# Optimization experiments

Measured on AMD Instinct MI355X. Metric: run time of the kernel, lower is better.

## Reference

```python
import jax, jax.numpy as jnp
import numpy as np

MARGIN_1 = 1.0
MARGIN_2 = 1.5
ALPHA_1 = 2.4
ALPHA_2 = 2.2
TVAL = 1.0
EPS = 1e-5


def setup_inputs() -> dict:
    key = jax.random.key(0)
    k1, k2, k3 = jax.random.split(key, 3)
    N, D = 4096, 2048
    x = jax.random.normal(k1, (N, D), dtype=jnp.float32)
    targets = jax.random.randint(k2, (N,), 0, 128, dtype=jnp.int32)
    sub = jax.random.randint(k3, (N,), 0, 2, dtype=jnp.int32)
    return {"x": x, "targets": targets, "sub": sub}


def _euclidean_dist(x):
    # pairwise distances of rows, clamped like torch .clamp(min=1e-12).sqrt()
    sq = jnp.sum(x * x, axis=1)  # [N]
    d2 = sq[:, None] + sq[None, :] - 2.0 * (x @ x.T)
    return jnp.sqrt(jnp.maximum(d2, 1e-12))  # [N, N]


def reference(x, targets, sub):
    # L2 normalize rows (norm=True path)
    x = x / jnp.maximum(jnp.linalg.norm(x, axis=1, keepdims=True), 1e-12)
    dist = _euclidean_dist(x)  # [N, N]
    N = dist.shape[0]

    eye = jnp.eye(N, dtype=bool)
    same_id = targets[:, None] == targets[None, :]
    is_pos = same_id & ~eye
    is_neg = ~same_id
    intra = sub[:, None] == sub[None, :]

    m_pos_intra = is_pos & intra
    m_pos_cross = is_pos & ~intra
    m_neg_intra = is_neg & intra
    m_neg_cross = is_neg & ~intra

    def ap_term(mask, margin, alpha):
        vals = jnp.maximum(dist + (margin - alpha), 0.0)
        cnt = jnp.sum(mask, axis=1).astype(dist.dtype)
        return jnp.sum(jnp.where(mask, vals, 0.0), axis=1) / (cnt + EPS)

    def an_term(mask, alpha):
        sel = mask & (dist < alpha)
        diff = alpha - dist  # = (alpha - d); weight = exp(tval * diff)
        w = jnp.where(sel, jnp.exp(TVAL * diff), 0.0)
        num = jnp.sum(jnp.where(sel, diff, 0.0) * w, axis=1)
        den = jnp.sum(w, axis=1) + EPS
        return num / den

    loss_rows = (
        ap_term(m_pos_intra, MARGIN_1, ALPHA_1)
        + ap_term(m_pos_cross, MARGIN_2, ALPHA_2)
        + an_term(m_neg_intra, ALPHA_1)
        + an_term(m_neg_cross, ALPHA_2)
    )
    return jnp.sum(loss_rows) / N
```

## Files before the change

### kernel.cpp

```cpp
#include <hip/hip_runtime.h>
#include <math.h>

#define THREADS 256
#define GT 512
#define BM 128
#define QBK 64
#define EPSV 1e-5f
#define C1E 11.023176380641601f
#define C2E 9.025013499434122f
#define FP8_SCALE 256.0f
#define INV_SCALE2 1.52587890625e-5f

typedef float f32x4 __attribute__((ext_vector_type(4)));

__launch_bounds__(THREADS)
__global__ void norm_conv_fp8_kernel(const float* __restrict__ x,
                                     unsigned char* __restrict__ xq, int D) {
    const int row = blockIdx.x;
    const float4* x4 = (const float4*)(x + (size_t)row * D);
    const int tid = threadIdx.x;

    float s = 0.f;
    for (int b = tid * 2; b * 4 < D; b += THREADS * 2) {
        float4 v0 = x4[b];
        float4 v1 = x4[b + 1];
        s += v0.x * v0.x + v0.y * v0.y + v0.z * v0.z + v0.w * v0.w
           + v1.x * v1.x + v1.y * v1.y + v1.z * v1.z + v1.w * v1.w;
    }
#pragma unroll
    for (int off = 32; off > 0; off >>= 1) s += __shfl_down(s, off, 64);
    __shared__ float red[THREADS / 64 + 1];
    if ((tid & 63) == 0) red[tid >> 6] = s;
    __syncthreads();
    if (tid == 0) {
        float tot = 0.f;
#pragma unroll
        for (int w = 0; w < THREADS / 64; ++w) tot += red[w];
        red[THREADS / 64] = FP8_SCALE / fmaxf(sqrtf(tot), 1e-12f);
    }
    __syncthreads();
    const float sc = red[THREADS / 64];

    int2* out = (int2*)(xq + (size_t)row * D);
    for (int b = tid * 2; b * 4 < D; b += THREADS * 2) {
        float4 v0 = x4[b];
        float4 v1 = x4[b + 1];
        int lo = __builtin_amdgcn_cvt_pk_fp8_f32(v0.x * sc, v0.y * sc, 0, 0);
        lo = __builtin_amdgcn_cvt_pk_fp8_f32(v0.z * sc, v0.w * sc, lo, 1);
        int hi = __builtin_amdgcn_cvt_pk_fp8_f32(v1.x * sc, v1.y * sc, 0, 0);
        hi = __builtin_amdgcn_cvt_pk_fp8_f32(v1.z * sc, v1.w * sc, hi, 1);
        int2 o; o.x = lo; o.y = hi;
        out[b >> 1] = o;
    }
}

__global__ void row_inv_norm_kernel(const float* __restrict__ x,
                                    float* __restrict__ inv_norm, int D) {
    const int row = blockIdx.x;
    const float4* x4 = (const float4*)(x + (size_t)row * D);
    const int nf4 = D >> 2;
    float s = 0.f;
    for (int i = threadIdx.x; i < nf4; i += THREADS) {
        float4 v = x4[i];
        s += v.x * v.x + v.y * v.y + v.z * v.z + v.w * v.w;
    }
#pragma unroll
    for (int off = 32; off > 0; off >>= 1) s += __shfl_down(s, off, 64);
    __shared__ float red[THREADS / 64];
    if ((threadIdx.x & 63) == 0) red[threadIdx.x >> 6] = s;
    __syncthreads();
    if (threadIdx.x == 0) {
        float tot = 0.f;
#pragma unroll
        for (int w = 0; w < THREADS / 64; ++w) tot += red[w];
        inv_norm[row] = 1.0f / fmaxf(sqrtf(tot), 1e-12f);
    }
}

#define GLDS16(g, l)                                                          \
    __builtin_amdgcn_global_load_lds(                                         \
        (const __attribute__((address_space(1))) unsigned int*)(g),           \
        (__attribute__((address_space(3))) unsigned int*)(l), 16, 0, 0)

__launch_bounds__(GT, 6)
__global__ void gram_fp8_kernel(const unsigned char* __restrict__ xq,
                                const int* __restrict__ targets,
                                const int* __restrict__ sub,
                                float* __restrict__ pr,
                                float* __restrict__ pc,
                                int D) {
    __shared__ unsigned char As[2][BM * QBK];
    __shared__ unsigned char Bs[2][BM * QBK];

    int tk = blockIdx.x;
    if ((gridDim.x & 7) == 0) {
        const int per = gridDim.x >> 3;
        tk = (tk & 7) * per + (tk >> 3);
    }

    int bx = (int)((sqrtf(8.0f * tk + 1.0f) - 1.0f) * 0.5f);
    while ((bx + 1) * (bx + 2) / 2 <= tk) ++bx;
    while (bx * (bx + 1) / 2 > tk) --bx;
    const int by = tk - bx * (bx + 1) / 2;

    const int tid = threadIdx.x;
    const int w = tid >> 6;
    const int lane = tid & 63;
    const int wm = w >> 2;
    const int wn = w & 3;
    const int quad = lane >> 4;
    const int cl = lane & 15;

    const int rowA0 = by * BM;
    const int colB0 = bx * BM;

    const int r0 = tid >> 2;
    const int qs = (tid & 3) ^ ((tid >> 3) & 3);
    const unsigned char* sA = xq + (size_t)(rowA0 + r0) * D + qs * 16;
    const unsigned char* sB = xq + (size_t)(colB0 + r0) * D + qs * 16;
    const int dof = w * 1024;

    int aoff[4], boff[2];
#pragma unroll
    for (int mi = 0; mi < 4; ++mi) {
        const int ar = wm * 64 + mi * 16 + cl;
        aoff[mi] = ar * QBK + ((((quad >> 1) ^ ((ar >> 1) & 3)) << 4))
                 + ((quad & 1) << 3);
    }
#pragma unroll
    for (int ni = 0; ni < 2; ++ni) {
        const int br = wn * 32 + ni * 16 + cl;
        boff[ni] = br * QBK + ((((quad >> 1) ^ ((br >> 1) & 3)) << 4))
                 + ((quad & 1) << 3);
    }

    f32x4 accv[4][2];
#pragma unroll
    for (int mi = 0; mi < 4; ++mi)
#pragma unroll
        for (int ni = 0; ni < 2; ++ni) accv[mi][ni] = (f32x4)(0.f);

    const int nIter = D / QBK;

    GLDS16(sA, &As[0][0] + dof);
    GLDS16(sB, &Bs[0][0] + dof);
    __syncthreads();

    for (int it = 0; it < nIter; ++it) {
        const int cur = it & 1;
        const int nxt = cur ^ 1;

        if (it + 1 < nIter) {
            const int kb = (it + 1) * QBK;
            GLDS16(sA + kb, &As[nxt][0] + dof);
            GLDS16(sB + kb, &Bs[nxt][0] + dof);
        }

        long af[4], bfv[2];
#pragma unroll
        for (int mi = 0; mi < 4; ++mi)
            af[mi] = *(const long*)&As[cur][aoff[mi]];
#pragma unroll
        for (int ni = 0; ni < 2; ++ni)
            bfv[ni] = *(const long*)&Bs[cur][boff[ni]];
#pragma unroll
        for (int mi = 0; mi < 4; ++mi)
#pragma unroll
            for (int ni = 0; ni < 2; ++ni)
                accv[mi][ni] = __builtin_amdgcn_mfma_f32_16x16x32_fp8_fp8(
                    af[mi], bfv[ni], accv[mi][ni], 0, 0, 0);
#pragma unroll
        for (int mi = 0; mi < 4; ++mi)
            af[mi] = *(const long*)&As[cur][aoff[mi] ^ 32];
#pragma unroll
        for (int ni = 0; ni < 2; ++ni)
            bfv[ni] = *(const long*)&Bs[cur][boff[ni] ^ 32];
#pragma unroll
        for (int mi = 0; mi < 4; ++mi)
#pragma unroll
            for (int ni = 0; ni < 2; ++ni)
                accv[mi][ni] = __builtin_amdgcn_mfma_f32_16x16x32_fp8_fp8(
                    af[mi], bfv[ni], accv[mi][ni], 0, 0, 0);

        __syncthreads();
    }

    int tj[2], sj[2];
#pragma unroll
    for (int ni = 0; ni < 2; ++ni) {
        const int gc = colB0 + wn * 32 + ni * 16 + cl;
        tj[ni] = targets[gc];
        sj[ni] = sub[gc];
    }

    float* rowp = (float*)&As[0][0];
#pragma unroll
    for (int mi = 0; mi < 4; ++mi) {
#pragma unroll
        for (int r = 0; r < 4; ++r) {
            const int rloc = wm * 64 + mi * 16 + quad * 4 + r;
            const int gi = rowA0 + rloc;
            const int ti = targets[gi];
            const int si = sub[gi];

            float s0 = 0.f, s1 = 0.f, s2 = 0.f, s3 = 0.f;
            float s4 = 0.f, s5 = 0.f, s6 = 0.f, s7 = 0.f;
#pragma unroll
            for (int ni = 0; ni < 2; ++ni) {
                const int gj = colB0 + wn * 32 + ni * 16 + cl;
                const float d2 =
                    fmaf(-2.0f * INV_SCALE2, accv[mi][ni][r], 2.0f);
                const float dd = sqrtf(fmaxf(d2, 1e-12f));
                accv[mi][ni][r] = dd;
                const bool same = (ti == tj[ni]);
                const bool intra = (si == sj[ni]);
                const bool pos = same && (gi != gj);
                const bool neg = !same;
                const float mg = intra ? 1.4f : 0.7f;
                const float v = fmaxf(dd - mg, 0.f);
                const float e = __expf(-dd);
                const float de = dd * e;
                if (pos && intra)  { s0 += v;  s1 += 1.f; }
                if (pos && !intra) { s2 += v;  s3 += 1.f; }
                if (neg && intra)  { s4 += de; s5 += e; }
                if (neg && !intra) { s6 += de; s7 += e; }
            }
#pragma unroll
            for (int off = 1; off < 16; off <<= 1) {
                s0 += __shfl_xor(s0, off, 64);
                s1 += __shfl_xor(s1, off, 64);
                s2 += __shfl_xor(s2, off, 64);
                s3 += __shfl_xor(s3, off, 64);
                s4 += __shfl_xor(s4, off, 64);
                s5 += __shfl_xor(s5, off, 64);
                s6 += __shfl_xor(s6, off, 64);
                s7 += __shfl_xor(s7, off, 64);
            }
            if (cl == 0) {
                float* dst = rowp + ((wn << 7) + rloc) * 8;
                float4 p0 = {s0, s1, s2, s3};
                float4 p1 = {s4, s5, s6, s7};
                *(float4*)(dst) = p0;
                *(float4*)(dst + 4) = p1;
            }
        }
    }
    __syncthreads();
    {
        const size_t prbase = (size_t)tk * 1024;
        for (int i = tid; i < 1024; i += GT)
            pr[prbase + i] = rowp[i] + rowp[1024 + i]
                           + rowp[2048 + i] + rowp[3072 + i];
    }

    float* colp = (float*)&Bs[0][0];
#pragma unroll
    for (int ni = 0; ni < 2; ++ni) {
        const int gj = colB0 + wn * 32 + ni * 16 + cl;
        const int tjc = tj[ni];
        const int sjc = sj[ni];
        float s0 = 0.f, s1 = 0.f, s2 = 0.f, s3 = 0.f;
        float s4 = 0.f, s5 = 0.f, s6 = 0.f, s7 = 0.f;
#pragma unroll
        for (int mi = 0; mi < 4; ++mi) {
#pragma unroll
            for (int r = 0; r < 4; ++r) {
                const int gi = rowA0 + wm * 64 + mi * 16 + quad * 4 + r;
                const int ti = targets[gi];
                const int si = sub[gi];
                const float dd = accv[mi][ni][r];
                const bool same = (ti == tjc);
                const bool intra = (si == sjc);
                const bool pos = same && (gi != gj);
                const bool neg = !same;
                const float mg = intra ? 1.4f : 0.7f;
                const float v = fmaxf(dd - mg, 0.f);
                const float e = __expf(-dd);
                const float de = dd * e;
                if (pos && intra)  { s0 += v;  s1 += 1.f; }
                if (pos && !intra) { s2 += v;  s3 += 1.f; }
                if (neg && intra)  { s4 += de; s5 += e; }
                if (neg && !intra) { s6 += de; s7 += e; }
            }
        }
        s0 += __shfl_xor(s0, 16, 64); s0 += __shfl_xor(s0, 32, 64);
        s1 += __shfl_xor(s1, 16, 64); s1 += __shfl_xor(s1, 32, 64);
        s2 += __shfl_xor(s2, 16, 64); s2 += __shfl_xor(s2, 32, 64);
        s3 += __shfl_xor(s3, 16, 64); s3 += __shfl_xor(s3, 32, 64);
        s4 += __shfl_xor(s4, 16, 64); s4 += __shfl_xor(s4, 32, 64);
        s5 += __shfl_xor(s5, 16, 64); s5 += __shfl_xor(s5, 32, 64);
        s6 += __shfl_xor(s6, 16, 64); s6 += __shfl_xor(s6, 32, 64);
        s7 += __shfl_xor(s7, 16, 64); s7 += __shfl_xor(s7, 32, 64);
        if (lane < 16) {
            const int colloc = wn * 32 + ni * 16 + lane;
            float* dst = colp + ((wm << 7) + colloc) * 8;
            float4 p0 = {s0, s1, s2, s3};
            float4 p1 = {s4, s5, s6, s7};
            *(float4*)(dst) = p0;
            *(float4*)(dst + 4) = p1;
        }
    }
    __syncthreads();
    {
        const float om = (bx == by) ? 0.f : 1.f;
        const size_t pcbase = (size_t)tk * 1024;
        for (int i = tid; i < 1024; i += GT)
            pc[pcbase + i] = (colp[i] + colp[1024 + i]) * om;
    }
}

__global__ void finalize_sym_kernel(const float* __restrict__ pr,
                                    const float* __restrict__ pc,
                                    float* __restrict__ out, int N, int nbx) {
    const int tid = threadIdx.x;
    const int rloc16 = tid >> 4;
    const int st = tid & 15;
    const int i = blockIdx.x * 16 + rloc16;
    const int B = i >> 7;
    const int rl = i & 127;
    const int nrow = nbx - B;
    const int ntot = nbx + 1;

    float a0 = 0.f, a1 = 0.f, a2 = 0.f, a3 = 0.f;
    float a4 = 0.f, a5 = 0.f, a6 = 0.f, a7 = 0.f;
    for (int s = st; s < ntot; s += 16) {
        const float* base;
        if (s < nrow) {
            const int bxx = B + s;
            base = pr + ((size_t)(bxx * (bxx + 1) / 2 + B) * 128 + rl) * 8;
        } else {
            const int byy = s - nrow;
            base = pc + ((size_t)(B * (B + 1) / 2 + byy) * 128 + rl) * 8;
        }
        float4 u0 = *(const float4*)(base);
        float4 u1 = *(const float4*)(base + 4);
        a0 += u0.x; a1 += u0.y; a2 += u0.z; a3 += u0.w;
        a4 += u1.x; a5 += u1.y; a6 += u1.z; a7 += u1.w;
    }
#pragma unroll
    for (int off = 1; off < 16; off <<= 1) {
        a0 += __shfl_xor(a0, off, 64);
        a1 += __shfl_xor(a1, off, 64);
        a2 += __shfl_xor(a2, off, 64);
        a3 += __shfl_xor(a3, off, 64);
        a4 += __shfl_xor(a4, off, 64);
        a5 += __shfl_xor(a5, off, 64);
        a6 += __shfl_xor(a6, off, 64);
        a7 += __shfl_xor(a7, off, 64);
    }
    __shared__ float lred[16];
    if (st == 0) {
        const float l = a0 / (a1 + EPSV) + a2 / (a3 + EPSV)
            + (C1E * fmaf(2.4f, a5, -a4)) / (C1E * a5 + EPSV)
            + (C2E * fmaf(2.2f, a7, -a6)) / (C2E * a7 + EPSV);
        lred[rloc16] = l;
    }
    __syncthreads();
    if (tid == 0) {
        float tot = 0.f;
#pragma unroll
        for (int k2 = 0; k2 < 16; ++k2) tot += lred[k2];
        atomicAdd(out, tot / (float)N);
    }
}

__launch_bounds__(THREADS, 2)
__global__ void dist_loss_kernel(const float* __restrict__ x,
                                 const int* __restrict__ targets,
                                 const int* __restrict__ sub,
                                 const float* __restrict__ inv_norm,
                                 float* __restrict__ acc,
                                 int N, int D) {
    __shared__ float Asf[16][128];
    __shared__ float Bsf[16][128];

    const int nbx = N / 128;
    const int bx = blockIdx.x % nbx;
    const int by = blockIdx.x / nbx;
    const int tid = threadIdx.x;
    const int tx = tid & 15;
    const int ty = tid >> 4;
    const int rowA0 = by * 128;
    const int colB0 = bx * 128;
    const float* Abase = x + (size_t)rowA0 * D;
    const float* Bbase = x + (size_t)colB0 * D;

    float accv[8][8];
#pragma unroll
    for (int r = 0; r < 8; ++r)
#pragma unroll
        for (int c = 0; c < 8; ++c) accv[r][c] = 0.f;

    for (int kb = 0; kb < D; kb += 16) {
#pragma unroll
        for (int l = 0; l < 2; ++l) {
            const int f = tid + l * THREADS;
            const int row = f >> 2;
            const int kq = (f & 3) << 2;
            float4 va = *(const float4*)(Abase + (size_t)row * D + kb + kq);
            float4 vb = *(const float4*)(Bbase + (size_t)row * D + kb + kq);
            Asf[kq + 0][row] = va.x; Asf[kq + 1][row] = va.y;
            Asf[kq + 2][row] = va.z; Asf[kq + 3][row] = va.w;
            Bsf[kq + 0][row] = vb.x; Bsf[kq + 1][row] = vb.y;
            Bsf[kq + 2][row] = vb.z; Bsf[kq + 3][row] = vb.w;
        }
        __syncthreads();
#pragma unroll
        for (int k = 0; k < 16; ++k) {
            float4 a0 = *(const float4*)&Asf[k][ty * 8];
            float4 a1 = *(const float4*)&Asf[k][ty * 8 + 4];
            float4 b0 = *(const float4*)&Bsf[k][tx * 8];
            float4 b1 = *(const float4*)&Bsf[k][tx * 8 + 4];
            float ar[8] = {a0.x, a0.y, a0.z, a0.w, a1.x, a1.y, a1.z, a1.w};
            float br[8] = {b0.x, b0.y, b0.z, b0.w, b1.x, b1.y, b1.z, b1.w};
#pragma unroll
            for (int r = 0; r < 8; ++r)
#pragma unroll
                for (int c = 0; c < 8; ++c)
                    accv[r][c] = fmaf(ar[r], br[c], accv[r][c]);
        }
        __syncthreads();
    }

    const int row_base = rowA0 + ty * 8;
    const int col_base = colB0 + tx * 8;
    int tjc[8], sjc[8];
    float invj[8];
#pragma unroll
    for (int c = 0; c < 8; ++c) {
        tjc[c] = targets[col_base + c];
        sjc[c] = sub[col_base + c];
        invj[c] = inv_norm[col_base + c];
    }
#pragma unroll
    for (int r = 0; r < 8; ++r) {
        const int gi = row_base + r;
        const int ti = targets[gi];
        const int si = sub[gi];
        const float invi = inv_norm[gi];
        float s0 = 0.f, s1 = 0.f, s2 = 0.f, s3 = 0.f;
        float s4 = 0.f, s5 = 0.f, s6 = 0.f, s7 = 0.f;
#pragma unroll
        for (int c = 0; c < 8; ++c) {
            const int gj = col_base + c;
            const float dot = accv[r][c] * invi * invj[c];
            const float dd = sqrtf(fmaxf(2.f - 2.f * dot, 1e-12f));
            const bool same = (ti == tjc[c]);
            const bool intra = (si == sjc[c]);
            const bool pos = same && (gi != gj);
            const bool neg = !same;
            const float df = (intra ? 2.4f : 2.2f) - dd;
            const float wgt = __expf(df);
            const float v = fmaxf(dd - (intra ? 1.4f : 0.7f), 0.f);
            if (pos && intra)  { s0 += v; s1 += 1.f; }
            if (pos && !intra) { s2 += v; s3 += 1.f; }
            if (neg && intra)  { s4 += df * wgt; s5 += wgt; }
            if (neg && !intra) { s6 += df * wgt; s7 += wgt; }
        }
#pragma unroll
        for (int off = 1; off < 16; off <<= 1) {
            s0 += __shfl_xor(s0, off, 64);
            s1 += __shfl_xor(s1, off, 64);
            s2 += __shfl_xor(s2, off, 64);
            s3 += __shfl_xor(s3, off, 64);
            s4 += __shfl_xor(s4, off, 64);
            s5 += __shfl_xor(s5, off, 64);
            s6 += __shfl_xor(s6, off, 64);
            s7 += __shfl_xor(s7, off, 64);
        }
        if (tx == 0) {
            float* a = acc + (size_t)gi * 8;
            atomicAdd(a + 0, s0); atomicAdd(a + 1, s1);
            atomicAdd(a + 2, s2); atomicAdd(a + 3, s3);
            atomicAdd(a + 4, s4); atomicAdd(a + 5, s5);
            atomicAdd(a + 6, s6); atomicAdd(a + 7, s7);
        }
    }
}

__global__ void finalize_kernel(const float* __restrict__ acc,
                                float* __restrict__ out, int N) {
    float s = 0.f;
    for (int i = threadIdx.x; i < N; i += THREADS) {
        const float* a = acc + (size_t)i * 8;
        s += a[0] / (a[1] + EPSV) + a[2] / (a[3] + EPSV)
           + a[4] / (a[5] + EPSV) + a[6] / (a[7] + EPSV);
    }
#pragma unroll
    for (int off = 32; off > 0; off >>= 1) s += __shfl_down(s, off, 64);
    __shared__ float red[THREADS / 64];
    if ((threadIdx.x & 63) == 0) red[threadIdx.x >> 6] = s;
    __syncthreads();
    if (threadIdx.x == 0) {
        float tot = 0.f;
#pragma unroll
        for (int w = 0; w < THREADS / 64; ++w) tot += red[w];
        out[0] = tot / (float)N;
    }
}

extern "C" void kernel_launch(void* const* d_in, const int* in_sizes, int n_in,
                              void* d_out, int out_size, void* d_ws, size_t ws_size,
                              hipStream_t stream) {
    const float* x = (const float*)d_in[0];
    const int* targets = (const int*)d_in[1];
    const int* sub = (const int*)d_in[2];
    const int N = in_sizes[1];
    const int D = in_sizes[0] / N;

    const int nbx = N / BM;
    const int T = nbx * (nbx + 1) / 2;
    const size_t sliceB = (size_t)T * 128 * 8 * sizeof(float);
    const size_t need = (size_t)N * D + 2 * sliceB;

    if (ws_size >= need) {
        unsigned char* xq = (unsigned char*)d_ws;
        float* pr = (float*)((char*)d_ws + (size_t)N * D);
        float* pc = pr + (size_t)T * 128 * 8;

        hipMemsetAsync(d_out, 0, sizeof(float), stream);
        norm_conv_fp8_kernel<<<N, THREADS, 0, stream>>>(x, xq, D);
        gram_fp8_kernel<<<T, GT, 0, stream>>>(xq, targets, sub, pr, pc, D);
        finalize_sym_kernel<<<N / 16, THREADS, 0, stream>>>(
            pr, pc, (float*)d_out, N, nbx);
    } else {
        float* inv_norm = (float*)d_ws;
        float* acc = inv_norm + N;
        hipMemsetAsync(acc, 0, (size_t)N * 8 * sizeof(float), stream);
        row_inv_norm_kernel<<<N, THREADS, 0, stream>>>(x, inv_norm, D);
        dist_loss_kernel<<<nbx * nbx, THREADS, 0, stream>>>(
            x, targets, sub, inv_norm, acc, N, D);
        finalize_kernel<<<1, THREADS, 0, stream>>>(acc, (float*)d_out, N);
    }
}
```

Measured before the change: 179.7 us.

## Use 4-wave 64x64 warp tiles with triple-buffered LDS and vmcnt-based pipelining

The fp8 Gram kernel drops from 8 waves to 4 waves per 128x128 tile, so each wave computes a 64x64 sub-tile (4x4 MFMA blocks), which raises register reuse of the A/B fragments. The LDS ring grows from double to triple buffering, with loads issued two stages ahead and synchronised by explicit s_waitcnt vmcnt plus a barrier, replacing the per-iteration __syncthreads. Row targets and sub values are preloaded into registers once. The cost is more accumulator registers per thread and lower occupancy (launch bounds 256 threads, 3 blocks per CU), and the hand-written waitcnt assumes a fixed count of outstanding loads.

```diff
diff --git a/kernel.cpp b/kernel.cpp
--- a/kernel.cpp
+++ b/kernel.cpp
@@ -2,7 +2,6 @@
 #include <math.h>
 
 #define THREADS 256
-#define GT 512
 #define BM 128
 #define QBK 64
 #define EPSV 1e-5f
@@ -82,15 +81,15 @@
         (const __attribute__((address_space(1))) unsigned int*)(g),           \
         (__attribute__((address_space(3))) unsigned int*)(l), 16, 0, 0)
 
-__launch_bounds__(GT, 6)
+__launch_bounds__(THREADS, 3)
 __global__ void gram_fp8_kernel(const unsigned char* __restrict__ xq,
                                 const int* __restrict__ targets,
                                 const int* __restrict__ sub,
                                 float* __restrict__ pr,
                                 float* __restrict__ pc,
                                 int D) {
-    __shared__ unsigned char As[2][BM * QBK];
-    __shared__ unsigned char Bs[2][BM * QBK];
+    __shared__ unsigned char As[3][BM * QBK];
+    __shared__ unsigned char Bs[3][BM * QBK];
 
     int tk = blockIdx.x;
     if ((gridDim.x & 7) == 0) {
@@ -106,91 +105,122 @@
     const int tid = threadIdx.x;
     const int w = tid >> 6;
     const int lane = tid & 63;
-    const int wm = w >> 2;
-    const int wn = w & 3;
+    const int wm = w >> 1;
+    const int wn = w & 1;
     const int quad = lane >> 4;
     const int cl = lane & 15;
 
     const int rowA0 = by * BM;
     const int colB0 = bx * BM;
 
-    const int r0 = tid >> 2;
     const int qs = (tid & 3) ^ ((tid >> 3) & 3);
-    const unsigned char* sA = xq + (size_t)(rowA0 + r0) * D + qs * 16;
-    const unsigned char* sB = xq + (size_t)(colB0 + r0) * D + qs * 16;
-    const int dof = w * 1024;
-
-    int aoff[4], boff[2];
+    const unsigned char* sA[2];
+    const unsigned char* sB[2];
+    int dof[2];
+#pragma unroll
+    for (int l = 0; l < 2; ++l) {
+        const int r = l * 64 + (tid >> 2);
+        sA[l] = xq + (size_t)(rowA0 + r) * D + qs * 16;
+        sB[l] = xq + (size_t)(colB0 + r) * D + qs * 16;
+        dof[l] = (l * 256 + w * 64) * 16;
+    }
+
+    int aoff[4], boff[4];
 #pragma unroll
     for (int mi = 0; mi < 4; ++mi) {
         const int ar = wm * 64 + mi * 16 + cl;
-        aoff[mi] = ar * QBK + ((((quad >> 1) ^ ((ar >> 1) & 3)) << 4))
+        aoff[mi] = ar * QBK + (((quad >> 1) ^ ((ar >> 1) & 3)) << 4)
                  + ((quad & 1) << 3);
     }
 #pragma unroll
-    for (int ni = 0; ni < 2; ++ni) {
-        const int br = wn * 32 + ni * 16 + cl;
-        boff[ni] = br * QBK + ((((quad >> 1) ^ ((br >> 1) & 3)) << 4))
+    for (int ni = 0; ni < 4; ++ni) {
+        const int br = wn * 64 + ni * 16 + cl;
+        boff[ni] = br * QBK + (((quad >> 1) ^ ((br >> 1) & 3)) << 4)
                  + ((quad & 1) << 3);
     }
 
-    f32x4 accv[4][2];
+    f32x4 accv[4][4];
 #pragma unroll
     for (int mi = 0; mi < 4; ++mi)
 #pragma unroll
-        for (int ni = 0; ni < 2; ++ni) accv[mi][ni] = (f32x4)(0.f);
+        for (int ni = 0; ni < 4; ++ni) accv[mi][ni] = (f32x4)(0.f);
 
     const int nIter = D / QBK;
 
-    GLDS16(sA, &As[0][0] + dof);
-    GLDS16(sB, &Bs[0][0] + dof);
-    __syncthreads();
-
-    for (int it = 0; it < nIter; ++it) {
-        const int cur = it & 1;
-        const int nxt = cur ^ 1;
-
-        if (it + 1 < nIter) {
-            const int kb = (it + 1) * QBK;
-            GLDS16(sA + kb, &As[nxt][0] + dof);
-            GLDS16(sB + kb, &Bs[nxt][0] + dof);
-        }
-
-        long af[4], bfv[2];
+#pragma unroll
+    for (int l = 0; l < 2; ++l) {
+        GLDS16(sA[l], &As[0][0] + dof[l]);
+        GLDS16(sB[l], &Bs[0][0] + dof[l]);
+    }
+#pragma unroll
+    for (int l = 0; l < 2; ++l) {
+        GLDS16(sA[l] + QBK, &As[1][0] + dof[l]);
+        GLDS16(sB[l] + QBK, &Bs[1][0] + dof[l]);
+    }
+
+    int cs = 0;
+    int ps = 2;
+    for (int t = 0; t < nIter; ++t) {
+        if (t + 1 < nIter)
+            asm volatile("s_waitcnt vmcnt(4)" ::: "memory");
+        else
+            asm volatile("s_waitcnt vmcnt(0)" ::: "memory");
+        __builtin_amdgcn_s_barrier();
+
+        if (t + 2 < nIter) {
+            const int kb = (t + 2) * QBK;
+#pragma unroll
+            for (int l = 0; l < 2; ++l) {
+                GLDS16(sA[l] + kb, &As[ps][0] + dof[l]);
+                GLDS16(sB[l] + kb, &Bs[ps][0] + dof[l]);
+            }
+        }
+
+        const unsigned char* Ac = &As[cs][0];
+        const unsigned char* Bc = &Bs[cs][0];
+        long af[4], bf[4];
 #pragma unroll
         for (int mi = 0; mi < 4; ++mi)
-            af[mi] = *(const long*)&As[cur][aoff[mi]];
-#pragma unroll
-        for (int ni = 0; ni < 2; ++ni)
-            bfv[ni] = *(const long*)&Bs[cur][boff[ni]];
+            af[mi] = *(const long*)(Ac + aoff[mi]);
+#pragma unroll
+        for (int ni = 0; ni < 4; ++ni)
+            bf[ni] = *(const long*)(Bc + boff[ni]);
 #pragma unroll
         for (int mi = 0; mi < 4; ++mi)
 #pragma unroll
-            for (int ni = 0; ni < 2; ++ni)
+            for (int ni = 0; ni < 4; ++ni)
                 accv[mi][ni] = __builtin_amdgcn_mfma_f32_16x16x32_fp8_fp8(
-                    af[mi], bfv[ni], accv[mi][ni], 0, 0, 0);
+                    af[mi], bf[ni], accv[mi][ni], 0, 0, 0);
 #pragma unroll
         for (int mi = 0; mi < 4; ++mi)
-            af[mi] = *(const long*)&As[cur][aoff[mi] ^ 32];
-#pragma unroll
-        for (int ni = 0; ni < 2; ++ni)
-            bfv[ni] = *(const long*)&Bs[cur][boff[ni] ^ 32];
+            af[mi] = *(const long*)(Ac + (aoff[mi] ^ 32));
+#pragma unroll
+        for (int ni = 0; ni < 4; ++ni)
+            bf[ni] = *(const long*)(Bc + (boff[ni] ^ 32));
 #pragma unroll
         for (int mi = 0; mi < 4; ++mi)
 #pragma unroll
-            for (int ni = 0; ni < 2; ++ni)
+            for (int ni = 0; ni < 4; ++ni)
                 accv[mi][ni] = __builtin_amdgcn_mfma_f32_16x16x32_fp8_fp8(
-                    af[mi], bfv[ni], accv[mi][ni], 0, 0, 0);
-
-        __syncthreads();
-    }
-
-    int tj[2], sj[2];
-#pragma unroll
-    for (int ni = 0; ni < 2; ++ni) {
-        const int gc = colB0 + wn * 32 + ni * 16 + cl;
+                    af[mi], bf[ni], accv[mi][ni], 0, 0, 0);
+
+        cs = (cs == 2) ? 0 : cs + 1;
+        ps = (ps == 2) ? 0 : ps + 1;
+    }
+
+    int tj[4], sj[4];
+#pragma unroll
+    for (int ni = 0; ni < 4; ++ni) {
+        const int gc = colB0 + wn * 64 + ni * 16 + cl;
         tj[ni] = targets[gc];
         sj[ni] = sub[gc];
+    }
+    int tiv[16], siv[16];
+#pragma unroll
+    for (int k = 0; k < 16; ++k) {
+        const int gi = rowA0 + wm * 64 + (k >> 2) * 16 + quad * 4 + (k & 3);
+        tiv[k] = targets[gi];
+        siv[k] = sub[gi];
     }
 
     float* rowp = (float*)&As[0][0];
@@ -200,14 +230,14 @@
         for (int r = 0; r < 4; ++r) {
             const int rloc = wm * 64 + mi * 16 + quad * 4 + r;
             const int gi = rowA0 + rloc;
-            const int ti = targets[gi];
-            const int si = sub[gi];
+            const int ti = tiv[mi * 4 + r];
+            const int si = siv[mi * 4 + r];
 
             float s0 = 0.f, s1 = 0.f, s2 = 0.f, s3 = 0.f;
             float s4 = 0.f, s5 = 0.f, s6 = 0.f, s7 = 0.f;
 #pragma unroll
-            for (int ni = 0; ni < 2; ++ni) {
-                const int gj = colB0 + wn * 32 + ni * 16 + cl;
+            for (int ni = 0; ni < 4; ++ni) {
+                const int gj = colB0 + wn * 64 + ni * 16 + cl;
                 const float d2 =
                     fmaf(-2.0f * INV_SCALE2, accv[mi][ni][r], 2.0f);
                 const float dd = sqrtf(fmaxf(d2, 1e-12f));
@@ -248,15 +278,14 @@
     __syncthreads();
     {
         const size_t prbase = (size_t)tk * 1024;
-        for (int i = tid; i < 1024; i += GT)
-            pr[prbase + i] = rowp[i] + rowp[1024 + i]
-                           + rowp[2048 + i] + rowp[3072 + i];
+        for (int i = tid; i < 1024; i += THREADS)
+            pr[prbase + i] = rowp[i] + rowp[1024 + i];
     }
 
     float* colp = (float*)&Bs[0][0];
 #pragma unroll
-    for (int ni = 0; ni < 2; ++ni) {
-        const int gj = colB0 + wn * 32 + ni * 16 + cl;
+    for (int ni = 0; ni < 4; ++ni) {
+        const int gj = colB0 + wn * 64 + ni * 16 + cl;
         const int tjc = tj[ni];
         const int sjc = sj[ni];
         float s0 = 0.f, s1 = 0.f, s2 = 0.f, s3 = 0.f;
@@ -266,8 +295,8 @@
 #pragma unroll
             for (int r = 0; r < 4; ++r) {
                 const int gi = rowA0 + wm * 64 + mi * 16 + quad * 4 + r;
-                const int ti = targets[gi];
-                const int si = sub[gi];
+                const int ti = tiv[mi * 4 + r];
+                const int si = siv[mi * 4 + r];
                 const float dd = accv[mi][ni][r];
                 const bool same = (ti == tjc);
                 const bool intra = (si == sjc);
@@ -292,7 +321,7 @@
         s6 += __shfl_xor(s6, 16, 64); s6 += __shfl_xor(s6, 32, 64);
         s7 += __shfl_xor(s7, 16, 64); s7 += __shfl_xor(s7, 32, 64);
         if (lane < 16) {
-            const int colloc = wn * 32 + ni * 16 + lane;
+            const int colloc = wn * 64 + ni * 16 + lane;
             float* dst = colp + ((wm << 7) + colloc) * 8;
             float4 p0 = {s0, s1, s2, s3};
             float4 p1 = {s4, s5, s6, s7};
@@ -304,7 +333,7 @@
     {
         const float om = (bx == by) ? 0.f : 1.f;
         const size_t pcbase = (size_t)tk * 1024;
-        for (int i = tid; i < 1024; i += GT)
+        for (int i = tid; i < 1024; i += THREADS)
             pc[pcbase + i] = (colp[i] + colp[1024 + i]) * om;
     }
 }
@@ -520,7 +549,8 @@
 
         hipMemsetAsync(d_out, 0, sizeof(float), stream);
         norm_conv_fp8_kernel<<<N, THREADS, 0, stream>>>(x, xq, D);
-        gram_fp8_kernel<<<T, GT, 0, stream>>>(xq, targets, sub, pr, pc, D);
+        gram_fp8_kernel<<<T, THREADS, 0, stream>>>(xq, targets, sub,
+                                                   pr, pc, D);
         finalize_sym_kernel<<<N / 16, THREADS, 0, stream>>>(
             pr, pc, (float*)d_out, N, nbx);
     } else {
```

Result: faster. 164.6 us (-8.4%).
